# Kernel optimization log

Hardware: AMD Instinct MI355X
Metric: run time of the kernel (lower is better)

## Reference

```python
import jax, jax.numpy as jnp
import numpy as np

B, N, D, H, E, W, OUT = 4, 2048, 128, 4, 32768, 8, 128


def setup_inputs() -> dict:
    key = jax.random.key(0)
    ks = jax.random.split(key, 11)
    s = 0.05  # weight init scale
    return {
        "nodefeatures": jax.random.normal(ks[0], (B, N, D), jnp.float32),
        "node_indices": jax.random.randint(ks[1], (B, 2, E), 0, N),
        "nodeattributes": jax.random.uniform(ks[2], (B, E, W), jnp.float32),
        "wq_w": jax.random.normal(ks[3], (H, D, D), jnp.float32) * s,
        "wq_b": jax.random.normal(ks[4], (H, D), jnp.float32) * s,
        "wk_w": jax.random.normal(ks[5], (H, D, D), jnp.float32) * s,
        "wk_b": jax.random.normal(ks[6], (H, D), jnp.float32) * s,
        "wv_w": jax.random.normal(ks[7], (H, D, D), jnp.float32) * s,
        "wv_b": jax.random.normal(ks[8], (H, D), jnp.float32) * s,
        "out_w": jax.random.normal(ks[9], (OUT, H * D), jnp.float32) * s,
        "out_b": jax.random.normal(ks[10], (OUT,), jnp.float32) * s,
    }


def reference(nodefeatures, node_indices, nodeattributes,
              wq_w, wq_b, wk_w, wk_b, wv_w, wv_b, out_w, out_b):
    b, n, d = nodefeatures.shape
    h = wq_w.shape[0]
    # per-head Linear projections: y = x @ W.T + bias, batched over heads -> [b,h,n,d]
    q = jnp.einsum('bnd,hed->bhne', nodefeatures, wq_w) + wq_b[None, :, None, :]
    k = jnp.einsum('bnd,hed->bhne', nodefeatures, wk_w) + wk_b[None, :, None, :]
    v = jnp.einsum('bnd,hed->bhne', nodefeatures, wv_w) + wv_b[None, :, None, :]

    i = node_indices[:, 0, :]  # [b,E] row indices
    j = node_indices[:, 1, :]  # [b,E] col indices

    # gather q_i, k_j per edge -> [b,h,E,d]; edge score = <q_i,k_j>/sqrt(n)
    qi = jnp.take_along_axis(q, i[:, None, :, None], axis=2)
    kj = jnp.take_along_axis(k, j[:, None, :, None], axis=2)
    wsum = nodeattributes.sum(axis=-1)  # [b,E] (x_edge[:,None]*weights).sum(1)
    # original divides by k.shape[1]**0.5 == sqrt(n)
    edge = (qi * kj).sum(-1) / (n ** 0.5) * wsum[:, None, :]  # [b,h,E]

    # scatter edge scores into zero-initialized dense logits [b,h,n,n]
    bi = jnp.arange(b)[:, None, None]
    hi = jnp.arange(h)[None, :, None]
    scores = jnp.zeros((b, h, n, n), q.dtype).at[bi, hi, i[:, None, :], j[:, None, :]].set(edge)

    attn = jax.nn.softmax(scores, axis=-1)
    o = jnp.einsum('bhnm,bhmd->bhnd', attn, v)
    o = o.transpose(0, 2, 1, 3).reshape(b, n, h * d)  # concat heads on feature dim
    return o @ out_w.T + out_b
```

## Files before the change

### kernel.cpp

```cpp
#include <hip/hip_runtime.h>
#include <hip/hip_bf16.h>
#include <math.h>

constexpr int B_ = 4;
constexpr int N_ = 2048;
constexpr int D_ = 128;
constexpr int H_ = 4;
constexpr int E_ = 32768;
constexpr int W_ = 8;
constexpr int OUT_ = 128;
constexpr int HD_ = H_ * D_;
constexpr int C3_ = 3 * HD_;
constexpr int CAP = 64;
constexpr int M_ = B_ * N_;

typedef __attribute__((ext_vector_type(8))) __bf16 bf16x8;
typedef __attribute__((ext_vector_type(4))) float f32x4;
typedef unsigned int uint32;
typedef unsigned short u16;

__device__ __forceinline__ u16 f2b(float f) {
    __hip_bfloat16 h = __float2bfloat16(f);
    return *(u16*)&h;
}
__device__ __forceinline__ float blo(uint32 u) { return __uint_as_float(u << 16); }
__device__ __forceinline__ float bhi(uint32 u) { return __uint_as_float(u & 0xffff0000u); }

__device__ __forceinline__ void g2l16(const void* g, void* l) {
    __builtin_amdgcn_global_load_lds(
        (const __attribute__((address_space(1))) unsigned int*)(uintptr_t)g,
        (__attribute__((address_space(3))) unsigned int*)(uintptr_t)l,
        16, 0, 0);
}

__global__ __launch_bounds__(256) void prep_kernel(
    const float* __restrict__ X,
    const float* __restrict__ wq, const float* __restrict__ wk, const float* __restrict__ wv,
    const float* __restrict__ bq, const float* __restrict__ bk, const float* __restrict__ bv,
    const float* __restrict__ OW,
    const int* __restrict__ nidx, const float* __restrict__ attr,
    u16* __restrict__ Xbf, u16* __restrict__ Wbf, float* __restrict__ biasf,
    u16* __restrict__ OWbf,
    int* __restrict__ row_count, int2* __restrict__ row_edges)
{
    const int blk = blockIdx.x;
    if (blk < 512) {
        const int tid = blk * 256 + threadIdx.x;
        const int row = tid >> 4, sub = tid & 15;
        const float4 f0 = *(const float4*)(X + (size_t)row * 128 + sub * 8);
        const float4 f1 = *(const float4*)(X + (size_t)row * 128 + sub * 8 + 4);
        union { u16 u[8]; uint4 v; } pk;
        pk.u[0]=f2b(f0.x); pk.u[1]=f2b(f0.y); pk.u[2]=f2b(f0.z); pk.u[3]=f2b(f0.w);
        pk.u[4]=f2b(f1.x); pk.u[5]=f2b(f1.y); pk.u[6]=f2b(f1.z); pk.u[7]=f2b(f1.w);
        const int ob = row * 256 + ((sub * 16) ^ ((row & 7) << 4));
        *(uint4*)((char*)Xbf + ob) = pk.v;
    } else if (blk < 608) {
        const int c = (blk - 512) * 256 + threadIdx.x;
        const int g = c >> 11, idx = c & 2047;
        const int t3 = g >> 2, h = g & 3;
        const float* Wsrc = (t3 == 0 ? wq : t3 == 1 ? wk : wv) + (size_t)h * 128 * 128;
        const int e = idx >> 4, sub = idx & 15;
        const float4 f0 = *(const float4*)(Wsrc + (size_t)e * 128 + sub * 8);
        const float4 f1 = *(const float4*)(Wsrc + (size_t)e * 128 + sub * 8 + 4);
        union { u16 u[8]; uint4 v; } pk;
        pk.u[0]=f2b(f0.x); pk.u[1]=f2b(f0.y); pk.u[2]=f2b(f0.z); pk.u[3]=f2b(f0.w);
        pk.u[4]=f2b(f1.x); pk.u[5]=f2b(f1.y); pk.u[6]=f2b(f1.z); pk.u[7]=f2b(f1.w);
        const int ob = g * 32768 + e * 256 + ((sub * 16) ^ ((e & 7) << 4));
        *(uint4*)((char*)Wbf + ob) = pk.v;
        if (idx < 128) {
            const float* Bsrc = (t3 == 0 ? bq : t3 == 1 ? bk : bv) + h * 128;
            biasf[g * 128 + idx] = Bsrc[idx];
        }
    } else if (blk < 640) {
        const int tid = (blk - 608) * 256 + threadIdx.x;
        const int c = tid >> 6, sub = tid & 63;
        const float4 f0 = *(const float4*)(OW + (size_t)c * 512 + sub * 8);
        const float4 f1 = *(const float4*)(OW + (size_t)c * 512 + sub * 8 + 4);
        union { u16 u[8]; uint4 v; } pk;
        pk.u[0]=f2b(f0.x); pk.u[1]=f2b(f0.y); pk.u[2]=f2b(f0.z); pk.u[3]=f2b(f0.w);
        pk.u[4]=f2b(f1.x); pk.u[5]=f2b(f1.y); pk.u[6]=f2b(f1.z); pk.u[7]=f2b(f1.w);
        const int ob = c * 1024 + ((sub * 16) ^ ((c & 7) << 4));
        *(uint4*)((char*)OWbf + ob) = pk.v;
    } else {
        const int wave = threadIdx.x >> 6;
        const int lane = threadIdx.x & 63;
        const int gw = (blk - 640) * 4 + wave;
        const int e0g = gw * 8;
        const int b = e0g / E_;
        const int e0 = e0g % E_;

        float a = attr[((size_t)b * E_ + e0) * W_ + lane];
        a += __shfl_xor(a, 1);
        a += __shfl_xor(a, 2);
        a += __shfl_xor(a, 4);

        if ((lane & 7) == 0) {
            const int sub = lane >> 3;
            const int e = e0 + sub;
            const int i = nidx[b * 2 * E_ + e];
            const int j = nidx[b * 2 * E_ + E_ + e];
            const int pos = atomicAdd(&row_count[b * N_ + i], 1);
            if (pos < CAP)
                row_edges[(size_t)(b * N_ + i) * CAP + pos] =
                    make_int2(e | (j << 16), __float_as_int(a));
        }
    }
}

__global__ __launch_bounds__(256) void qkv_mfma(
    const u16* __restrict__ Xbf, const u16* __restrict__ Wbf,
    const float* __restrict__ biasf, u16* __restrict__ QKV,
    float* __restrict__ vsum)
{
    __shared__ u16 As[128 * 128];
    __shared__ u16 Bs[128 * 128];
    const int rb = blockIdx.x & 63;
    const int g  = blockIdx.x >> 6;
    const int t = threadIdx.x;
    const int lane = t & 63, wave = t >> 6;
    const int wm = wave >> 1, wn = wave & 1;
    const int l15 = lane & 15, l4 = lane >> 4;

    const char* Asrc = (const char*)(Xbf + (size_t)rb * 128 * 128);
    const char* Bsrc = (const char*)(Wbf + (size_t)g  * 128 * 128);
    #pragma unroll
    for (int q = 0; q < 8; ++q) {
        const int o = t * 16 + q * 4096;
        g2l16(Asrc + o, (char*)As + o);
        g2l16(Bsrc + o, (char*)Bs + o);
    }
    __syncthreads();

    f32x4 acc[4][4];
    #pragma unroll
    for (int i = 0; i < 4; ++i)
        #pragma unroll
        for (int j = 0; j < 4; ++j) acc[i][j] = (f32x4){0.f, 0.f, 0.f, 0.f};

    #pragma unroll
    for (int ks = 0; ks < 4; ++ks) {
        const int kb = ks * 64 + l4 * 16;
        bf16x8 a[4], bb[4];
        #pragma unroll
        for (int fm = 0; fm < 4; ++fm) {
            const int row = wm * 64 + fm * 16 + l15;
            a[fm] = *(const bf16x8*)((const char*)As + row * 256 + (kb ^ ((row & 7) << 4)));
        }
        #pragma unroll
        for (int fn = 0; fn < 4; ++fn) {
            const int col = wn * 64 + fn * 16 + l15;
            bb[fn] = *(const bf16x8*)((const char*)Bs + col * 256 + (kb ^ ((col & 7) << 4)));
        }
        #pragma unroll
        for (int fm = 0; fm < 4; ++fm)
            #pragma unroll
            for (int fn = 0; fn < 4; ++fn)
                acc[fm][fn] = __builtin_amdgcn_mfma_f32_16x16x32_bf16(
                    a[fm], bb[fn], acc[fm][fn], 0, 0, 0);
    }

    #pragma unroll
    for (int fm = 0; fm < 4; ++fm)
        #pragma unroll
        for (int fn = 0; fn < 4; ++fn) {
            const int col = wn * 64 + fn * 16 + l15;
            const float bv = biasf[g * 128 + col];
            const int gcol = g * 128 + col;
            #pragma unroll
            for (int r = 0; r < 4; ++r) {
                const int row = rb * 128 + wm * 64 + fm * 16 + l4 * 4 + r;
                QKV[(size_t)row * C3_ + gcol] = f2b(acc[fm][fn][r] + bv);
            }
        }

    if (g >= 8) {
        const int h = g - 8;
        const int b = rb >> 4;
        #pragma unroll
        for (int fn = 0; fn < 4; ++fn) {
            float s = 0.f;
            #pragma unroll
            for (int fm = 0; fm < 4; ++fm)
                #pragma unroll
                for (int r = 0; r < 4; ++r) s += acc[fm][fn][r];
            s += __shfl_xor(s, 16);
            s += __shfl_xor(s, 32);
            if (l4 == 0) {
                const int col = wn * 64 + fn * 16 + l15;
                const float bv = biasf[g * 128 + col];
                atomicAdd(&vsum[(b * H_ + h) * 128 + col], s + 64.f * bv);
            }
        }
    }
}

__global__ __launch_bounds__(256) void row_fused(
    const u16* __restrict__ QKV, const float* __restrict__ vsum,
    const int* __restrict__ row_count, const int2* __restrict__ row_edges,
    u16* __restrict__ Obf)
{
    const int t = threadIdx.x;
    const int wave = t >> 6, lane = t & 63;
    const int row = blockIdx.x * 4 + wave;
    const int b = blockIdx.y;
    const int R = b * N_ + row;
    int cnt = row_count[R];
    if (cnt > CAP) cnt = CAP;

    int ej = 0; float ws = 0.f;
    if (lane < cnt) {
        const int2 v = row_edges[(size_t)R * CAP + lane];
        ej = v.x; ws = __int_as_float(v.y);
    }
    const int myj = ej >> 16, mye = ej & 0xFFFF;
    bool win = (lane < cnt);
    for (int p = 0; p < cnt; ++p) {
        const int oj = __shfl(ej, p);
        if (win && (oj >> 16) == myj && (oj & 0xFFFF) > mye) win = false;
    }
    unsigned long long mask = __ballot(win);

    const char* base = (const char*)QKV;
    const uint4 qv = *(const uint4*)(base + (size_t)R * 3072 + lane * 16);
    const float q0=blo(qv.x), q1=bhi(qv.x), q2=blo(qv.y), q3=bhi(qv.y),
                q4=blo(qv.z), q5=bhi(qv.z), q6=blo(qv.w), q7=bhi(qv.w);
    const float rs = 0.02209708691207961f;

    float a0=0.f,a1=0.f,a2=0.f,a3=0.f,a4=0.f,a5=0.f,a6=0.f,a7=0.f;
    float dsum = 0.f;

    while (mask) {
        const int p = (int)__ffsll((long long)mask) - 1;
        mask &= mask - 1;
        const int j = __shfl(ej, p) >> 16;
        const float wsp = __shfl(ws, p);
        const char* nb = base + (size_t)(b * N_ + j) * 3072;
        const uint4 kv = *(const uint4*)(nb + 1024 + lane * 16);
        const uint4 vv = *(const uint4*)(nb + 2048 + lane * 16);
        float s = q0*blo(kv.x) + q1*bhi(kv.x) + q2*blo(kv.y) + q3*bhi(kv.y)
                + q4*blo(kv.z) + q5*bhi(kv.z) + q6*blo(kv.w) + q7*bhi(kv.w);
        s += __shfl_xor(s, 1);
        s += __shfl_xor(s, 2);
        s += __shfl_xor(s, 4);
        s += __shfl_xor(s, 8);
        const float x = expf(s * rs * wsp) - 1.f;
        dsum += x;
        a0 = fmaf(x, blo(vv.x), a0); a1 = fmaf(x, bhi(vv.x), a1);
        a2 = fmaf(x, blo(vv.y), a2); a3 = fmaf(x, bhi(vv.y), a3);
        a4 = fmaf(x, blo(vv.z), a4); a5 = fmaf(x, bhi(vv.z), a5);
        a6 = fmaf(x, blo(vv.w), a6); a7 = fmaf(x, bhi(vv.w), a7);
    }

    const float inv = 1.0f / (2048.0f + dsum);
    const float* vsp = vsum + (b * H_ + (lane >> 4)) * 128 + (lane & 15) * 8;
    const float4 vs0 = *(const float4*)vsp;
    const float4 vs1 = *(const float4*)(vsp + 4);
    union { u16 u[8]; uint4 v; } o;
    o.u[0]=f2b((vs0.x+a0)*inv); o.u[1]=f2b((vs0.y+a1)*inv);
    o.u[2]=f2b((vs0.z+a2)*inv); o.u[3]=f2b((vs0.w+a3)*inv);
    o.u[4]=f2b((vs1.x+a4)*inv); o.u[5]=f2b((vs1.y+a5)*inv);
    o.u[6]=f2b((vs1.z+a6)*inv); o.u[7]=f2b((vs1.w+a7)*inv);
    const int ob = ((lane >> 4) << 8) + (((lane & 15) * 16) ^ ((R & 7) << 4));
    *(uint4*)((char*)Obf + (size_t)R * 1024 + ob) = o.v;
}

__global__ __launch_bounds__(256) void out_mfma(
    const u16* __restrict__ Obf, const u16* __restrict__ OWbf,
    const float* __restrict__ bo, float* __restrict__ Out)
{
    __shared__ u16 As[64 * 128];
    __shared__ u16 Bs[128 * 128];
    const int rb = blockIdx.x;
    const int t = threadIdx.x;
    const int lane = t & 63, wave = t >> 6;
    const int wm = wave >> 1, wn = wave & 1;
    const int l15 = lane & 15, l4 = lane >> 4;

    f32x4 acc[2][4];
    #pragma unroll
    for (int i = 0; i < 2; ++i)
        #pragma unroll
        for (int j = 0; j < 4; ++j) acc[i][j] = (f32x4){0.f, 0.f, 0.f, 0.f};

    for (int kc = 0; kc < 4; ++kc) {
        #pragma unroll
        for (int q = 0; q < 4; ++q) {
            const int o = t * 16 + q * 4096;
            const int arow = o >> 8, ob = o & 255;
            g2l16((const char*)Obf + (size_t)(rb * 64 + arow) * 1024 + kc * 256 + ob,
                  (char*)As + o);
        }
        #pragma unroll
        for (int q = 0; q < 8; ++q) {
            const int o = t * 16 + q * 4096;
            const int c = o >> 8, ob = o & 255;
            g2l16((const char*)OWbf + (size_t)c * 1024 + kc * 256 + ob,
                  (char*)Bs + o);
        }
        __syncthreads();
        #pragma unroll
        for (int ks = 0; ks < 4; ++ks) {
            const int kb = ks * 64 + l4 * 16;
            bf16x8 a[2], bb[4];
            #pragma unroll
            for (int fm = 0; fm < 2; ++fm) {
                const int row = wm * 32 + fm * 16 + l15;
                a[fm] = *(const bf16x8*)((const char*)As + row * 256 + (kb ^ ((row & 7) << 4)));
            }
            #pragma unroll
            for (int fn = 0; fn < 4; ++fn) {
                const int col = wn * 64 + fn * 16 + l15;
                bb[fn] = *(const bf16x8*)((const char*)Bs + col * 256 + (kb ^ ((col & 7) << 4)));
            }
            #pragma unroll
            for (int fm = 0; fm < 2; ++fm)
                #pragma unroll
                for (int fn = 0; fn < 4; ++fn)
                    acc[fm][fn] = __builtin_amdgcn_mfma_f32_16x16x32_bf16(
                        a[fm], bb[fn], acc[fm][fn], 0, 0, 0);
        }
        __syncthreads();
    }

    #pragma unroll
    for (int fm = 0; fm < 2; ++fm)
        #pragma unroll
        for (int fn = 0; fn < 4; ++fn) {
            const int col = wn * 64 + fn * 16 + l15;
            const float bv = bo[col];
            #pragma unroll
            for (int r = 0; r < 4; ++r) {
                const int row = rb * 64 + wm * 32 + fm * 16 + l4 * 4 + r;
                Out[(size_t)row * OUT_ + col] = acc[fm][fn][r] + bv;
            }
        }
}

extern "C" void kernel_launch(void* const* d_in, const int* in_sizes, int n_in,
                              void* d_out, int out_size, void* d_ws, size_t ws_size,
                              hipStream_t stream)
{
    const float* x     = (const float*)d_in[0];
    const int*   nidx  = (const int*)  d_in[1];
    const float* attr  = (const float*)d_in[2];
    const float* wq_w  = (const float*)d_in[3];
    const float* wq_b  = (const float*)d_in[4];
    const float* wk_w  = (const float*)d_in[5];
    const float* wk_b  = (const float*)d_in[6];
    const float* wv_w  = (const float*)d_in[7];
    const float* wv_b  = (const float*)d_in[8];
    const float* out_w = (const float*)d_in[9];
    const float* out_b = (const float*)d_in[10];
    float* out = (float*)d_out;

    char* ws = (char*)d_ws;
    size_t off = 0;
    auto alloc = [&](size_t bytes) -> char* {
        char* p = ws + off;
        off += (bytes + 255) & ~(size_t)255;
        return p;
    };
    u16*  Xbf  = (u16*)alloc((size_t)M_ * D_ * 2);
    u16*  Wbf  = (u16*)alloc((size_t)12 * D_ * D_ * 2);
    float* biasf = (float*)alloc((size_t)12 * D_ * 4);
    u16*  QKV  = (u16*)alloc((size_t)M_ * C3_ * 2);
    u16*  OWbf = (u16*)alloc((size_t)OUT_ * HD_ * 2);
    u16*  Obf  = (u16*)alloc((size_t)M_ * HD_ * 2);
    float* vsum = (float*)alloc((size_t)B_ * H_ * D_ * 4);
    int*  row_count = (int*)alloc((size_t)B_ * N_ * 4);
    int2* row_edges = (int2*)alloc((size_t)B_ * N_ * CAP * 8);

    hipMemsetAsync(row_count, 0, (size_t)B_ * N_ * 4, stream);
    hipMemsetAsync(vsum, 0, (size_t)B_ * H_ * D_ * 4, stream);

    prep_kernel<<<640 + (B_ * E_) / 32, 256, 0, stream>>>(
        x, wq_w, wk_w, wv_w, wq_b, wk_b, wv_b, out_w, nidx, attr,
        Xbf, Wbf, biasf, OWbf, row_count, row_edges);
    qkv_mfma<<<64 * 12, 256, 0, stream>>>(Xbf, Wbf, biasf, QKV, vsum);
    row_fused<<<dim3(N_ / 4, B_), 256, 0, stream>>>(
        QKV, vsum, row_count, row_edges, Obf);
    out_mfma<<<M_ / 64, 256, 0, stream>>>(Obf, OWbf, out_b, out);
}
```

Measured before the change: 87.79 us.

## Zero buffers in prep kernel, stage QKV stores through LDS, prefetch edge loads

The two memsets are replaced by one extra block in the prep kernel that zeroes row_count and vsum, and edge appending moves into its own kernel so it runs after the zeroing. The QKV GEMM epilogue now writes results into shared memory and then issues coalesced 16-byte global stores, replacing scattered 2-byte writes. The row_fused edge loop is software-pipelined so the K/V loads for the next edge are issued before the current edge is computed. Together these trade one memset-style launch for an extra kernel launch plus more LDS traffic and register use.

After: 84.24 us. -4.0%, faster.

```diff
diff --git a/kernel.cpp b/kernel.cpp
--- a/kernel.cpp
+++ b/kernel.cpp
@@ -38,10 +38,9 @@
     const float* __restrict__ wq, const float* __restrict__ wk, const float* __restrict__ wv,
     const float* __restrict__ bq, const float* __restrict__ bk, const float* __restrict__ bv,
     const float* __restrict__ OW,
-    const int* __restrict__ nidx, const float* __restrict__ attr,
     u16* __restrict__ Xbf, u16* __restrict__ Wbf, float* __restrict__ biasf,
     u16* __restrict__ OWbf,
-    int* __restrict__ row_count, int2* __restrict__ row_edges)
+    int* __restrict__ row_count, float* __restrict__ vsum)
 {
     const int blk = blockIdx.x;
     if (blk < 512) {
@@ -82,28 +81,41 @@
         const int ob = c * 1024 + ((sub * 16) ^ ((c & 7) << 4));
         *(uint4*)((char*)OWbf + ob) = pk.v;
     } else {
-        const int wave = threadIdx.x >> 6;
-        const int lane = threadIdx.x & 63;
-        const int gw = (blk - 640) * 4 + wave;
-        const int e0g = gw * 8;
-        const int b = e0g / E_;
-        const int e0 = e0g % E_;
-
-        float a = attr[((size_t)b * E_ + e0) * W_ + lane];
-        a += __shfl_xor(a, 1);
-        a += __shfl_xor(a, 2);
-        a += __shfl_xor(a, 4);
-
-        if ((lane & 7) == 0) {
-            const int sub = lane >> 3;
-            const int e = e0 + sub;
-            const int i = nidx[b * 2 * E_ + e];
-            const int j = nidx[b * 2 * E_ + E_ + e];
-            const int pos = atomicAdd(&row_count[b * N_ + i], 1);
-            if (pos < CAP)
-                row_edges[(size_t)(b * N_ + i) * CAP + pos] =
-                    make_int2(e | (j << 16), __float_as_int(a));
-        }
+        const uint4 z = make_uint4(0, 0, 0, 0);
+        uint4* rc = (uint4*)row_count;
+        #pragma unroll
+        for (int q = 0; q < 8; ++q) rc[threadIdx.x + q * 256] = z;
+        uint4* vs = (uint4*)vsum;
+        #pragma unroll
+        for (int q = 0; q < 2; ++q) vs[threadIdx.x + q * 256] = z;
+    }
+}
+
+__global__ __launch_bounds__(256) void append_kernel(
+    const int* __restrict__ nidx, const float* __restrict__ attr,
+    int* __restrict__ row_count, int2* __restrict__ row_edges)
+{
+    const int wave = threadIdx.x >> 6;
+    const int lane = threadIdx.x & 63;
+    const int gw = blockIdx.x * 4 + wave;
+    const int e0g = gw * 8;
+    const int b = e0g / E_;
+    const int e0 = e0g % E_;
+
+    float a = attr[((size_t)b * E_ + e0) * W_ + lane];
+    a += __shfl_xor(a, 1);
+    a += __shfl_xor(a, 2);
+    a += __shfl_xor(a, 4);
+
+    if ((lane & 7) == 0) {
+        const int sub = lane >> 3;
+        const int e = e0 + sub;
+        const int i = nidx[b * 2 * E_ + e];
+        const int j = nidx[b * 2 * E_ + E_ + e];
+        const int pos = atomicAdd(&row_count[b * N_ + i], 1);
+        if (pos < CAP)
+            row_edges[(size_t)(b * N_ + i) * CAP + pos] =
+                make_int2(e | (j << 16), __float_as_int(a));
     }
 }
 
@@ -159,17 +171,19 @@
                     a[fm], bb[fn], acc[fm][fn], 0, 0, 0);
     }
 
+    __syncthreads();
+
     #pragma unroll
     for (int fm = 0; fm < 4; ++fm)
         #pragma unroll
         for (int fn = 0; fn < 4; ++fn) {
             const int col = wn * 64 + fn * 16 + l15;
             const float bv = biasf[g * 128 + col];
-            const int gcol = g * 128 + col;
             #pragma unroll
             for (int r = 0; r < 4; ++r) {
-                const int row = rb * 128 + wm * 64 + fm * 16 + l4 * 4 + r;
-                QKV[(size_t)row * C3_ + gcol] = f2b(acc[fm][fn][r] + bv);
+                const int row = wm * 64 + fm * 16 + l4 * 4 + r;
+                *(u16*)((char*)As + row * 256 + ((col * 2) ^ ((row & 7) << 4))) =
+                    f2b(acc[fm][fn][r] + bv);
             }
         }
 
@@ -192,6 +206,15 @@
             }
         }
     }
+    __syncthreads();
+
+    #pragma unroll
+    for (int q = 0; q < 8; ++q) {
+        const int idx = t + q * 256;
+        const int row = idx >> 4, c = idx & 15;
+        const uint4 v = *(const uint4*)((char*)As + row * 256 + ((c * 16) ^ ((row & 7) << 4)));
+        *(uint4*)(QKV + (size_t)(rb * 128 + row) * C3_ + g * 128 + c * 8) = v;
+    }
 }
 
 __global__ __launch_bounds__(256) void row_fused(
@@ -218,7 +241,7 @@
         const int oj = __shfl(ej, p);
         if (win && (oj >> 16) == myj && (oj & 0xFFFF) > mye) win = false;
     }
-    unsigned long long mask = __ballot(win);
+    unsigned long long m = __ballot(win);
 
     const char* base = (const char*)QKV;
     const uint4 qv = *(const uint4*)(base + (size_t)R * 3072 + lane * 16);
@@ -229,27 +252,42 @@
     float a0=0.f,a1=0.f,a2=0.f,a3=0.f,a4=0.f,a5=0.f,a6=0.f,a7=0.f;
     float dsum = 0.f;
 
-    while (mask) {
-        const int p = (int)__ffsll((long long)mask) - 1;
-        mask &= mask - 1;
-        const int j = __shfl(ej, p) >> 16;
-        const float wsp = __shfl(ws, p);
-        const char* nb = base + (size_t)(b * N_ + j) * 3072;
-        const uint4 kv = *(const uint4*)(nb + 1024 + lane * 16);
-        const uint4 vv = *(const uint4*)(nb + 2048 + lane * 16);
-        float s = q0*blo(kv.x) + q1*bhi(kv.x) + q2*blo(kv.y) + q3*bhi(kv.y)
-                + q4*blo(kv.z) + q5*bhi(kv.z) + q6*blo(kv.w) + q7*bhi(kv.w);
-        s += __shfl_xor(s, 1);
-        s += __shfl_xor(s, 2);
-        s += __shfl_xor(s, 4);
-        s += __shfl_xor(s, 8);
-        const float x = expf(s * rs * wsp) - 1.f;
-        dsum += x;
-        a0 = fmaf(x, blo(vv.x), a0); a1 = fmaf(x, bhi(vv.x), a1);
-        a2 = fmaf(x, blo(vv.y), a2); a3 = fmaf(x, bhi(vv.y), a3);
-        a4 = fmaf(x, blo(vv.z), a4); a5 = fmaf(x, bhi(vv.z), a5);
-        a6 = fmaf(x, blo(vv.w), a6); a7 = fmaf(x, bhi(vv.w), a7);
-    }
+#define PROCESS(kv, vv, wsp)                                                  \
+    {                                                                         \
+        float s = q0*blo(kv.x) + q1*bhi(kv.x) + q2*blo(kv.y) + q3*bhi(kv.y)   \
+                + q4*blo(kv.z) + q5*bhi(kv.z) + q6*blo(kv.w) + q7*bhi(kv.w);  \
+        s += __shfl_xor(s, 1);                                                \
+        s += __shfl_xor(s, 2);                                                \
+        s += __shfl_xor(s, 4);                                                \
+        s += __shfl_xor(s, 8);                                                \
+        const float x = expf(s * rs * (wsp)) - 1.f;                           \
+        dsum += x;                                                            \
+        a0 = fmaf(x, blo(vv.x), a0); a1 = fmaf(x, bhi(vv.x), a1);             \
+        a2 = fmaf(x, blo(vv.y), a2); a3 = fmaf(x, bhi(vv.y), a3);             \
+        a4 = fmaf(x, blo(vv.z), a4); a5 = fmaf(x, bhi(vv.z), a5);             \
+        a6 = fmaf(x, blo(vv.w), a6); a7 = fmaf(x, bhi(vv.w), a7);             \
+    }
+
+    if (m) {
+        int p = (int)__ffsll(m) - 1; m &= m - 1;
+        int jc = __shfl(ej, p) >> 16;
+        float wc = __shfl(ws, p);
+        const char* nb = base + (size_t)(b * N_ + jc) * 3072;
+        uint4 kv = *(const uint4*)(nb + 1024 + lane * 16);
+        uint4 vv = *(const uint4*)(nb + 2048 + lane * 16);
+        while (m) {
+            const int p2 = (int)__ffsll(m) - 1; m &= m - 1;
+            const int j2 = __shfl(ej, p2) >> 16;
+            const float w2 = __shfl(ws, p2);
+            const char* nb2 = base + (size_t)(b * N_ + j2) * 3072;
+            const uint4 kv2 = *(const uint4*)(nb2 + 1024 + lane * 16);
+            const uint4 vv2 = *(const uint4*)(nb2 + 2048 + lane * 16);
+            PROCESS(kv, vv, wc);
+            kv = kv2; vv = vv2; wc = w2;
+        }
+        PROCESS(kv, vv, wc);
+    }
+#undef PROCESS
 
     const float inv = 1.0f / (2048.0f + dsum);
     const float* vsp = vsum + (b * H_ + (lane >> 4)) * 128 + (lane & 15) * 8;
@@ -370,12 +408,10 @@
     int*  row_count = (int*)alloc((size_t)B_ * N_ * 4);
     int2* row_edges = (int2*)alloc((size_t)B_ * N_ * CAP * 8);
 
-    hipMemsetAsync(row_count, 0, (size_t)B_ * N_ * 4, stream);
-    hipMemsetAsync(vsum, 0, (size_t)B_ * H_ * D_ * 4, stream);
-
-    prep_kernel<<<640 + (B_ * E_) / 32, 256, 0, stream>>>(
-        x, wq_w, wk_w, wv_w, wq_b, wk_b, wv_b, out_w, nidx, attr,
-        Xbf, Wbf, biasf, OWbf, row_count, row_edges);
+    prep_kernel<<<641, 256, 0, stream>>>(
+        x, wq_w, wk_w, wv_w, wq_b, wk_b, wv_b, out_w,
+        Xbf, Wbf, biasf, OWbf, row_count, vsum);
+    append_kernel<<<(B_ * E_) / 32, 256, 0, stream>>>(nidx, attr, row_count, row_edges);
     qkv_mfma<<<64 * 12, 256, 0, stream>>>(Xbf, Wbf, biasf, QKV, vsum);
     row_fused<<<dim3(N_ / 4, B_), 256, 0, stream>>>(
         QKV, vsum, row_count, row_edges, Obf);
```
